# Kernel tuning notes

Measured on AMD Instinct MI355X. Metric: run time of the kernel, lower is better.

## Reference

```python
import jax, jax.numpy as jnp
import numpy as np

DIM = 2048
N_HEADS = 16
HEAD_DIM = DIM // N_HEADS  # 128
B, T = 8, 1024


def setup_inputs() -> dict:
    key = jax.random.key(0)
    ks = jax.random.split(key, 5)
    s_in = 1.0 / np.sqrt(DIM)
    return {
        "x": jax.random.normal(ks[0], (B, T, DIM), dtype=jnp.float32),
        "W_qkv": jax.random.uniform(ks[1], (DIM + 2 * HEAD_DIM, DIM), dtype=jnp.float32, minval=-s_in, maxval=s_in),
        "b_qkv": jax.random.uniform(ks[2], (DIM + 2 * HEAD_DIM,), dtype=jnp.float32, minval=-s_in, maxval=s_in),
        "W_out": jax.random.uniform(ks[3], (DIM, DIM), dtype=jnp.float32, minval=-s_in, maxval=s_in),
        "b_out": jax.random.uniform(ks[4], (DIM,), dtype=jnp.float32, minval=-s_in, maxval=s_in),
    }


def reference(x, W_qkv, b_qkv, W_out, b_out):
    Bx, Tx, D = x.shape
    H, hd = N_HEADS, HEAD_DIM
    qkv = x @ W_qkv.T + b_qkv                      # [B,T,D+2*hd]
    q = qkv[:, :, :D].reshape(Bx, Tx, H, hd).transpose(0, 2, 1, 3)  # [B,H,T,hd]
    k = qkv[:, :, D:D + hd]                        # [B,T,hd] (shared head)
    v = qkv[:, :, D + hd:]                         # [B,T,hd]
    # torch repeat(1,1,H).view(B,T,H,hd) duplicates the single KV head -> broadcast instead
    scores = jnp.einsum('bhtd,bsd->bhts', q, k) / jnp.sqrt(jnp.asarray(hd, x.dtype))
    causal = jnp.tril(jnp.ones((Tx, Tx), dtype=bool))
    scores = jnp.where(causal[None, None], scores, jnp.asarray(-jnp.inf, x.dtype))
    att = jax.nn.softmax(scores, axis=-1)          # [B,H,T,T]
    out = jnp.einsum('bhts,bsd->bhtd', att, v)     # [B,H,T,hd]
    out = out.transpose(0, 2, 1, 3).reshape(Bx, Tx, D)
    return out @ W_out.T + b_out
```

## Files before the change

### kernel.cpp

```cpp
#include <hip/hip_runtime.h>
#include <hip/hip_bf16.h>
#include <math.h>
#include <stdint.h>

#define DIM 2048
#define NH 16
#define HD 128
#define BB 8
#define TT 1024
#define NROW (BB*TT)
#define QKVD (DIM + 2*HD)

typedef unsigned short u16;
typedef unsigned int u32;
typedef float f32x4 __attribute__((ext_vector_type(4)));
typedef u32 u32x4 __attribute__((ext_vector_type(4)));
typedef __bf16 bf16x8 __attribute__((ext_vector_type(8)));

#define QSCALE_LOG2E (0.08838834764831845f * 1.4426950408889634f)

__device__ inline u16 f2bf(float f) {
  u32 u = __builtin_bit_cast(u32, f);
  u += 0x7FFF + ((u >> 16) & 1);
  return (u16)(u >> 16);
}

__device__ inline u32 cvt_pk_bf16(float lo, float hi) {
  u32 d;
  asm("v_cvt_pk_bf16_f32 %0, %1, %2" : "=v"(d) : "v"(lo), "v"(hi));
  return d;
}

__device__ inline void gload_lds16(const void* g, void* l) {
  __builtin_amdgcn_global_load_lds(
      (const __attribute__((address_space(1))) void*)g,
      (__attribute__((address_space(3))) void*)l,
      16, 0, 0);
}

__global__ void cvt_f32_bf16(const float* __restrict__ in, u16* __restrict__ out, int n4) {
  int i = blockIdx.x * blockDim.x + threadIdx.x;
  int st = gridDim.x * blockDim.x;
  for (; i < n4; i += st) {
    float4 v = reinterpret_cast<const float4*>(in)[i];
    ushort4 o;
    o.x = f2bf(v.x); o.y = f2bf(v.y); o.z = f2bf(v.z); o.w = f2bf(v.w);
    reinterpret_cast<ushort4*>(out)[i] = o;
  }
}

template<bool OUT_BF16, bool WRITE_VT>
__global__ __launch_bounds__(256, 2) void gemm_nt(
    const u16* __restrict__ A, const u16* __restrict__ Bm,
    const float* __restrict__ bias, void* __restrict__ Cout,
    u16* __restrict__ vT, int K, int Mcols)
{
  __shared__ u16 As[128*32];
  __shared__ u16 Bs[128*32];
  const int tid = threadIdx.x;
  const int w = tid >> 6, l = tid & 63;
  const int wm = w >> 1, wn = w & 1;
  const int rl = l & 15, gl = l >> 4;
  const int rowBase = blockIdx.x * 128;
  const int colBase = blockIdx.y * 128;

  f32x4 acc[4][4] = {};

  for (int k0 = 0; k0 < K; k0 += 32) {
    __syncthreads();
#pragma unroll
    for (int i = 0; i < 2; ++i) {
      int c = i*256 + w*64 + l;
      int r = c >> 2, kc = c & 3;
      gload_lds16(A  + (size_t)(rowBase + r)*K + k0 + kc*8, &As[(i*256 + w*64)*8]);
      gload_lds16(Bm + (size_t)(colBase + r)*K + k0 + kc*8, &Bs[(i*256 + w*64)*8]);
    }
    __syncthreads();

    bf16x8 af[4], bf[4];
#pragma unroll
    for (int fm = 0; fm < 4; ++fm)
      af[fm] = *(const bf16x8*)&As[(wm*64 + fm*16 + rl)*32 + gl*8];
#pragma unroll
    for (int fn = 0; fn < 4; ++fn)
      bf[fn] = *(const bf16x8*)&Bs[(wn*64 + fn*16 + rl)*32 + gl*8];
#pragma unroll
    for (int fm = 0; fm < 4; ++fm)
#pragma unroll
      for (int fn = 0; fn < 4; ++fn)
        acc[fm][fn] = __builtin_amdgcn_mfma_f32_16x16x32_bf16(af[fm], bf[fn], acc[fm][fn], 0, 0, 0);
  }

  float bv[4];
#pragma unroll
  for (int fn = 0; fn < 4; ++fn) bv[fn] = bias[colBase + wn*64 + fn*16 + rl];

#pragma unroll
  for (int fm = 0; fm < 4; ++fm) {
#pragma unroll
    for (int fn = 0; fn < 4; ++fn) {
      const int col = colBase + wn*64 + fn*16 + rl;
#pragma unroll
      for (int r = 0; r < 4; ++r) {
        const int row = rowBase + wm*64 + fm*16 + gl*4 + r;
        float v = acc[fm][fn][r] + bv[fn];
        if (WRITE_VT && col >= DIM + HD) {
          int d = col - (DIM + HD);
          int b = row >> 10, t = row & 1023;
          vT[((size_t)(b*HD + d) << 10) + t] = f2bf(v);
        }
        float vs = (WRITE_VT && col < DIM) ? v * QSCALE_LOG2E : v;
        if (OUT_BF16) ((u16*)Cout)[(size_t)row*Mcols + col] = f2bf(vs);
        else          ((float*)Cout)[(size_t)row*Mcols + col] = vs;
      }
    }
  }
}

__global__ __launch_bounds__(512, 4) void mqa_attn(
    const u16* __restrict__ qkv, const u16* __restrict__ vT,
    u16* __restrict__ attout)
{
  __shared__ char lds[65536];

  const int tid = threadIdx.x;
  const int wid = tid >> 6, l = tid & 63;
  const int rl = l & 15, gl = l >> 4;
  const int qb = (int)gridDim.x - 1 - (int)blockIdx.x;
  const int b = blockIdx.y >> 4, h = blockIdx.y & 15;
  const int qrow0 = qb*128 + wid*16;
  const int diag = qrow0 >> 6;
  const int itmax = 2*qb + 1;

  const u16* kbase = qkv + (size_t)b*TT*QKVD + DIM;
  const u16* vbase = vT + ((size_t)b*HD << 10);

  auto STAGE = [&](int buf, int s0) {
    char* kl = lds + buf*32768;
    char* vl = kl + 16384;
#pragma unroll
    for (int i = 0; i < 2; ++i) {
      int L = (i*8 + wid)*1024 + l*16;
      int s = L >> 8, kb = (L & 255) ^ ((s & 7) << 4);
      gload_lds16(kbase + (size_t)(s0 + s)*QKVD + (kb >> 1), kl + (i*8 + wid)*1024);
      int d = L >> 7, sb = (L & 127) ^ ((d & 7) << 4);
      gload_lds16(vbase + ((size_t)d << 10) + s0 + (sb >> 1), vl + (i*8 + wid)*1024);
    }
  };

  STAGE(0, 0);
  asm volatile("" ::: "memory");

  bf16x8 qf[4];
  {
    const u16* qp = qkv + (size_t)(b*TT + qrow0 + rl)*QKVD + h*HD + gl*8;
#pragma unroll
    for (int kk = 0; kk < 4; ++kk) qf[kk] = *(const bf16x8*)(qp + kk*32);
  }

  f32x4 accO[8] = {};
  float mrow = -INFINITY, lrow = 0.f;
  const int tg = qrow0 + rl;
  const int addrA = (((gl & 1) * 2) * 16 + rl) * 4;
  const int addrB = addrA + 64;
  const bool hiSel = (gl >= 2);

  for (int it = 0; it <= itmax; ++it) {
    if (it < itmax) {
      STAGE((it + 1) & 1, (it + 1) << 6);
      asm volatile("s_waitcnt vmcnt(4)" ::: "memory");
    } else {
      asm volatile("s_waitcnt vmcnt(0)" ::: "memory");
    }
    __builtin_amdgcn_s_barrier();

    if (it <= diag) {
      const char* kl = lds + (it & 1)*32768;
      const char* vl = kl + 16384;

      f32x4 sc[4] = {};
      __builtin_amdgcn_s_setprio(1);
#pragma unroll
      for (int fs = 0; fs < 4; ++fs) {
        const int s = fs*16 + rl;
#pragma unroll
        for (int kkd = 0; kkd < 4; ++kkd) {
          bf16x8 kf = *(const bf16x8*)(kl + ((s*256 + kkd*64 + gl*16) ^ ((s & 7) << 4)));
          sc[fs] = __builtin_amdgcn_mfma_f32_16x16x32_bf16(kf, qf[kkd], sc[fs], 0, 0, 0);
        }
      }
      __builtin_amdgcn_s_setprio(0);

      if (it == diag) {
        const int s0 = it << 6;
#pragma unroll
        for (int fs = 0; fs < 4; ++fs)
#pragma unroll
          for (int r = 0; r < 4; ++r) {
            int sg = s0 + fs*16 + gl*4 + r;
            if (sg > tg) sc[fs][r] = -INFINITY;
          }
      }

      float mx = -INFINITY;
#pragma unroll
      for (int fs = 0; fs < 4; ++fs)
        mx = fmaxf(mx, fmaxf(fmaxf(sc[fs][0], sc[fs][1]), fmaxf(sc[fs][2], sc[fs][3])));
      mx = fmaxf(mx, __shfl_xor(mx, 16));
      mx = fmaxf(mx, __shfl_xor(mx, 32));

      if (!__all(mx <= mrow + 8.f)) {
        float mnew = fmaxf(mrow, mx);
        float rr = __builtin_amdgcn_exp2f(mrow - mnew);
#pragma unroll
        for (int fd = 0; fd < 8; ++fd)
#pragma unroll
          for (int r = 0; r < 4; ++r) accO[fd][r] *= rr;
        lrow *= rr;
        mrow = mnew;
      }

      float ps = 0.f;
#pragma unroll
      for (int fs = 0; fs < 4; ++fs)
#pragma unroll
        for (int r = 0; r < 4; ++r) {
          float p = __builtin_amdgcn_exp2f(sc[fs][r] - mrow);
          sc[fs][r] = p;
          ps += p;
        }
      ps += __shfl_xor(ps, 16);
      ps += __shfl_xor(ps, 32);
      lrow += ps;

      u32 pw[4][2];
#pragma unroll
      for (int fs = 0; fs < 4; ++fs) {
        pw[fs][0] = cvt_pk_bf16(sc[fs][0], sc[fs][1]);
        pw[fs][1] = cvt_pk_bf16(sc[fs][2], sc[fs][3]);
      }
      u32x4 bw[2];
#pragma unroll
      for (int kk = 0; kk < 2; ++kk)
#pragma unroll
        for (int w = 0; w < 4; ++w) {
          int addr = (w < 2) ? addrA : addrB;
          u32 lo = __builtin_amdgcn_ds_bpermute(addr, (int)pw[2*kk + 0][w & 1]);
          u32 hi = __builtin_amdgcn_ds_bpermute(addr, (int)pw[2*kk + 1][w & 1]);
          bw[kk][w] = hiSel ? hi : lo;
        }

      __builtin_amdgcn_s_setprio(1);
#pragma unroll
      for (int kk = 0; kk < 2; ++kk) {
        bf16x8 pb = __builtin_bit_cast(bf16x8, bw[kk]);
#pragma unroll
        for (int fd = 0; fd < 8; ++fd) {
          const int d = fd*16 + rl;
          bf16x8 vf = *(const bf16x8*)(vl + ((d*128 + kk*64 + gl*16) ^ ((d & 7) << 4)));
          accO[fd] = __builtin_amdgcn_mfma_f32_16x16x32_bf16(vf, pb, accO[fd], 0, 0, 0);
        }
      }
      __builtin_amdgcn_s_setprio(0);
    }

    __builtin_amdgcn_s_barrier();
  }

  const float inv = 1.0f / lrow;
  u16* outp = attout + (size_t)(b*TT + tg)*DIM + h*HD;
#pragma unroll
  for (int fd = 0; fd < 8; ++fd) {
    ushort4 o;
    o.x = f2bf(accO[fd][0] * inv);
    o.y = f2bf(accO[fd][1] * inv);
    o.z = f2bf(accO[fd][2] * inv);
    o.w = f2bf(accO[fd][3] * inv);
    *(ushort4*)(outp + fd*16 + gl*4) = o;
  }
}

extern "C" void kernel_launch(void* const* d_in, const int* in_sizes, int n_in,
                              void* d_out, int out_size, void* d_ws, size_t ws_size,
                              hipStream_t stream) {
  const float* x    = (const float*)d_in[0];
  const float* Wqkv = (const float*)d_in[1];
  const float* bqkv = (const float*)d_in[2];
  const float* Wout = (const float*)d_in[3];
  const float* bout = (const float*)d_in[4];

  char* ws = (char*)d_ws;
  u16* xb    = (u16*)(ws);
  u16* wqb   = (u16*)(ws + 33554432);
  u16* qkvb  = (u16*)(ws + 33554432 + 9437184);
  u16* vtb   = (u16*)(ws + 33554432 + 9437184 + 37748736);
  u16* attb  = xb;
  u16* woutb = wqb;

  cvt_f32_bf16<<<2048, 256, 0, stream>>>(x,    xb,  NROW*DIM/4);
  cvt_f32_bf16<<<2048, 256, 0, stream>>>(Wqkv, wqb, QKVD*DIM/4);

  dim3 g1(NROW/128, QKVD/128);
  gemm_nt<true, true><<<g1, 256, 0, stream>>>(xb, wqb, bqkv, qkvb, vtb, DIM, QKVD);

  cvt_f32_bf16<<<2048, 256, 0, stream>>>(Wout, woutb, DIM*DIM/4);

  dim3 ga(TT/128, BB*NH);
  mqa_attn<<<ga, 512, 0, stream>>>(qkvb, vtb, attb);

  dim3 g2(NROW/128, DIM/128);
  gemm_nt<false, false><<<g2, 256, 0, stream>>>(attb, woutb, bout, d_out, nullptr, DIM, DIM);
}
```

Before: 325.5 us.

## Triple-buffer GEMM LDS tiles with async prefetch and XOR swizzle

```diff
diff --git a/kernel.cpp b/kernel.cpp
--- a/kernel.cpp
+++ b/kernel.cpp
@@ -50,13 +50,12 @@
 }
 
 template<bool OUT_BF16, bool WRITE_VT>
-__global__ __launch_bounds__(256, 2) void gemm_nt(
+__global__ __launch_bounds__(256, 3) void gemm_nt(
     const u16* __restrict__ A, const u16* __restrict__ Bm,
     const float* __restrict__ bias, void* __restrict__ Cout,
     u16* __restrict__ vT, int K, int Mcols)
 {
-  __shared__ u16 As[128*32];
-  __shared__ u16 Bs[128*32];
+  __shared__ __align__(16) u16 sbuf[3][8192];
   const int tid = threadIdx.x;
   const int w = tid >> 6, l = tid & 63;
   const int wm = w >> 1, wn = w & 1;
@@ -64,32 +63,70 @@
   const int rowBase = blockIdx.x * 128;
   const int colBase = blockIdx.y * 128;
 
+  const int rT = tid >> 2;
+  const int t4 = tid & 3;
+  const int cswE = (t4 * 8) ^ (((rT >> 1) & 3) << 3);
+  const u16* aSrc0 = A  + (size_t)(rowBase + rT) * K + cswE;
+  const u16* bSrc0 = Bm + (size_t)(colBase + rT) * K + cswE;
+  const size_t rowSk = (size_t)64 * K;
+
+  auto STAGE = [&](int kt) {
+    u16* base = &sbuf[kt % 3][0];
+    const int k0 = kt * 32;
+    gload_lds16(aSrc0 + k0,         base + (size_t)tid * 8);
+    gload_lds16(aSrc0 + rowSk + k0, base + 2048 + (size_t)tid * 8);
+    gload_lds16(bSrc0 + k0,         base + 4096 + (size_t)tid * 8);
+    gload_lds16(bSrc0 + rowSk + k0, base + 4096 + 2048 + (size_t)tid * 8);
+  };
+
+  int aOff[4], bOff[4];
+#pragma unroll
+  for (int f = 0; f < 4; ++f) {
+    int ra = wm * 64 + f * 16 + rl;
+    aOff[f] = ra * 32 + ((gl * 8) ^ (((ra >> 1) & 3) << 3));
+    int rb = wn * 64 + f * 16 + rl;
+    bOff[f] = 4096 + rb * 32 + ((gl * 8) ^ (((rb >> 1) & 3) << 3));
+  }
+
   f32x4 acc[4][4] = {};
 
-  for (int k0 = 0; k0 < K; k0 += 32) {
-    __syncthreads();
-#pragma unroll
-    for (int i = 0; i < 2; ++i) {
-      int c = i*256 + w*64 + l;
-      int r = c >> 2, kc = c & 3;
-      gload_lds16(A  + (size_t)(rowBase + r)*K + k0 + kc*8, &As[(i*256 + w*64)*8]);
-      gload_lds16(Bm + (size_t)(colBase + r)*K + k0 + kc*8, &Bs[(i*256 + w*64)*8]);
-    }
-    __syncthreads();
-
-    bf16x8 af[4], bf[4];
-#pragma unroll
-    for (int fm = 0; fm < 4; ++fm)
-      af[fm] = *(const bf16x8*)&As[(wm*64 + fm*16 + rl)*32 + gl*8];
-#pragma unroll
-    for (int fn = 0; fn < 4; ++fn)
-      bf[fn] = *(const bf16x8*)&Bs[(wn*64 + fn*16 + rl)*32 + gl*8];
-#pragma unroll
-    for (int fm = 0; fm < 4; ++fm)
-#pragma unroll
-      for (int fn = 0; fn < 4; ++fn)
-        acc[fm][fn] = __builtin_amdgcn_mfma_f32_16x16x32_bf16(af[fm], bf[fn], acc[fm][fn], 0, 0, 0);
-  }
+#define GEMM_BODY(KT)                                                          \
+  {                                                                            \
+    __builtin_amdgcn_sched_barrier(0);                                         \
+    __builtin_amdgcn_s_barrier();                                              \
+    const u16* base = &sbuf[(KT) % 3][0];                                      \
+    bf16x8 af[4], bf[4];                                                       \
+    _Pragma("unroll")                                                          \
+    for (int f = 0; f < 4; ++f) af[f] = *(const bf16x8*)(base + aOff[f]);      \
+    _Pragma("unroll")                                                          \
+    for (int f = 0; f < 4; ++f) bf[f] = *(const bf16x8*)(base + bOff[f]);      \
+    asm volatile("s_waitcnt lgkmcnt(0)" ::: "memory");                         \
+    __builtin_amdgcn_sched_barrier(0);                                         \
+    __builtin_amdgcn_s_barrier();                                              \
+    __builtin_amdgcn_s_setprio(1);                                             \
+    _Pragma("unroll")                                                          \
+    for (int fm = 0; fm < 4; ++fm)                                             \
+      _Pragma("unroll")                                                        \
+      for (int fn = 0; fn < 4; ++fn)                                           \
+        acc[fm][fn] = __builtin_amdgcn_mfma_f32_16x16x32_bf16(af[fm], bf[fn],  \
+                                                              acc[fm][fn], 0, 0, 0); \
+    __builtin_amdgcn_s_setprio(0);                                             \
+  }
+
+  const int NT = K >> 5;
+  STAGE(0);
+  STAGE(1);
+
+  for (int kt = 0; kt < NT - 2; ++kt) {
+    STAGE(kt + 2);
+    asm volatile("s_waitcnt vmcnt(8)" ::: "memory");
+    GEMM_BODY(kt);
+  }
+  asm volatile("s_waitcnt vmcnt(4)" ::: "memory");
+  GEMM_BODY(NT - 2);
+  asm volatile("s_waitcnt vmcnt(0)" ::: "memory");
+  GEMM_BODY(NT - 1);
+#undef GEMM_BODY
 
   float bv[4];
 #pragma unroll
```

After: 305.9 us. -6.0%, faster.
